# Kernel optimization log

Hardware: AMD Instinct MI355X
Metric: run time of the kernel (lower is better)

## Reference

```python
import jax, jax.numpy as jnp
from jax import lax
import numpy as np

K = 3        # adaptive kernel size
STRIDE = 1
PAD = (K - 1) // 2


def setup_inputs() -> dict:
    key = jax.random.key(0)
    ks = jax.random.split(key, 10)
    N, C, H, W = 32, 512, 56, 56
    Cm, P = 128, 512  # Cm = inplanes // m, P = planes

    def rn(k, shape, scale=0.05):
        return jax.random.normal(k, shape, dtype=jnp.float32) * scale

    return dict(
        x=jax.random.normal(ks[0], (N, C, H, W), dtype=jnp.float32),
        conv_w=rn(ks[1], (Cm, C)),      # self.conv 1x1 weight (squeezed)
        conv_b=rn(ks[2], (Cm,)),        # self.conv bias
        ck_w=rn(ks[3], (K * K,)),       # self.conv_kernel 1x1 weight (1 in-ch)
        ck_b=rn(ks[4], (K * K,)),       # self.conv_kernel bias
        ckk_w=rn(ks[5], (Cm,)),         # self.conv_k 1x1 weight (1 in-ch)
        ckk_b=rn(ks[6], (Cm,)),         # self.conv_k bias
        adap_b=rn(ks[7], (Cm,)),        # self.conv_adap_kernel bias (weight is generated)
        fuse_w=rn(ks[8], (P, Cm)),      # self.fuse 1x1 weight (squeezed)
        fuse_b=rn(ks[9], (P,)),         # self.fuse bias
    )


def _forward(x, conv_w, conv_b, ck_w, ck_b, ckk_w, ckk_b, adap_b, fuse_w, fuse_b):
    N, C, H, W = x.shape
    Cm = conv_w.shape[0]

    # f = relu(conv(x)) : [N, Cm, H, W]
    f = jax.nn.relu(jnp.einsum('nchw,oc->nohw', x, conv_w) + conv_b[None, :, None, None])

    # g = relu(conv(avg_pool(x))) : [N, Cm]  (spatial dims are 1x1, squeezed)
    pooled = jnp.mean(x, axis=(2, 3))                       # [N, C]
    g = jax.nn.relu(pooled @ conv_w.T + conv_b)             # [N, Cm]

    # conv_kernel (1x1, 1->k*k channels) applied on permuted g:
    # ker[n, ic, kk] = ck_w[kk] * g[n, ic] + ck_b[kk]
    ker = g[:, :, None] * ck_w[None, None, :] + ck_b[None, None, :]   # [N, Cm, k*k]

    # conv_k (1x1, 1->Cm channels) generates per-sample dynamic conv weights:
    # Wk[n, oc, ic, kk] = relu(ckk_w[oc] * ker[n, ic, kk] + ckk_b[oc])
    Wk = jax.nn.relu(ckk_w[None, :, None, None] * ker[:, None, :, :]
                     + ckk_b[None, :, None, None])          # [N, Cm, Cm, k*k]
    Wk = Wk.reshape(N, Cm, Cm, K, K)                        # per-sample OIHW weights

    # Per-sample dynamic conv, batched with vmap (replaces the python loop + weight swap)
    def dyn_conv(f_n, w_n):  # f_n: [Cm,H,W], w_n: [Cm,Cm,K,K]
        return lax.conv_general_dilated(
            f_n[None], w_n, (STRIDE, STRIDE), [(PAD, PAD), (PAD, PAD)],
            dimension_numbers=('NCHW', 'OIHW', 'NCHW'))[0]

    y = jax.vmap(dyn_conv)(f, Wk) + adap_b[None, :, None, None]  # [N, Cm, H, W]

    # fuse 1x1 conv: Cm -> planes
    out = jnp.einsum('nchw,pc->nphw', y, fuse_w) + fuse_b[None, :, None, None]
    return out


def reference(x, conv_w, conv_b, ck_w, ck_b, ckk_w, ckk_b, adap_b, fuse_w, fuse_b):
    return _forward(x, conv_w, conv_b, ck_w, ck_b, ckk_w, ckk_b, adap_b, fuse_w, fuse_b)
```

## Files before the change

### kernel.cpp

```cpp
#include <hip/hip_runtime.h>

#define N_   32
#define C_   512
#define HW_  3136
#define W_   56
#define H_   56
#define CM_  128
#define P_   512

typedef __attribute__((ext_vector_type(8))) short bf16x8;
typedef __attribute__((ext_vector_type(4))) float f32x4;

__device__ inline ushort f2bf(float x) {
    unsigned u = __float_as_uint(x);
    u += 0x7fff + ((u >> 16) & 1);
    return (ushort)(u >> 16);
}

__global__ __launch_bounds__(256) void prep_w(const float* __restrict__ conv_w,
                                              const float* __restrict__ fuse_w,
                                              ushort* __restrict__ Acv,
                                              ushort* __restrict__ Afu,
                                              float* __restrict__ gacc) {
    int idx = blockIdx.x * 256 + threadIdx.x;
    if (idx < 4096) gacc[idx] = 0.f;
    if (idx < 65536) {
        int ci = idx & 7, cm = (idx >> 3) & 127, cb = idx >> 10;
        Acv[idx] = f2bf(conv_w[cm * C_ + cb * 8 + ci]);
    } else {
        int j = idx - 65536;
        int ci = j & 7, p = (j >> 3) & 511, kb = j >> 12;
        Afu[j] = f2bf(fuse_w[p * CM_ + kb * 8 + ci]);
    }
}

__global__ __launch_bounds__(256) void gemm_f(const float* __restrict__ x,
                                              const ushort* __restrict__ Acv,
                                              const float* __restrict__ conv_b,
                                              ushort* __restrict__ f_t,
                                              float* __restrict__ gacc) {
    int pixbase = blockIdx.x * 64, n = blockIdx.z;
    int t = threadIdx.x, wv = t >> 6, lane = t & 63, col = lane & 15, quad = lane >> 4;
    __shared__ ushort bsh[2][64 * 40];
    f32x4 z = {0.f, 0.f, 0.f, 0.f};
    f32x4 acc[2][4];
    #pragma unroll
    for (int mt = 0; mt < 2; mt++)
        #pragma unroll
        for (int ns = 0; ns < 4; ns++) acc[mt][ns] = z;

    int spix = t & 63, chq = wv * 8;
    const float* xb = &x[(size_t)n * C_ * HW_ + pixbase + spix];

    float v[8];
#define LOADV(c0)                                                              \
    {                                                                          \
        const float* xs = xb + (size_t)(c0) * HW_;                             \
        _Pragma("unroll")                                                      \
        for (int i = 0; i < 8; i++) v[i] = xs[(size_t)(chq + i) * HW_];        \
    }
#define PACKW(buf)                                                             \
    {                                                                          \
        unsigned p0 = (unsigned)f2bf(v[0]) | ((unsigned)f2bf(v[1]) << 16);     \
        unsigned p1 = (unsigned)f2bf(v[2]) | ((unsigned)f2bf(v[3]) << 16);     \
        unsigned p2 = (unsigned)f2bf(v[4]) | ((unsigned)f2bf(v[5]) << 16);     \
        unsigned p3 = (unsigned)f2bf(v[6]) | ((unsigned)f2bf(v[7]) << 16);     \
        *(uint4*)&bsh[buf][spix * 40 + chq] = make_uint4(p0, p1, p2, p3);      \
    }

    LOADV(0);
    PACKW(0);
    __syncthreads();
    int cur = 0;
    for (int cb0 = 0; cb0 < 16; cb0++) {
        if (cb0 < 15) {
            LOADV((cb0 + 1) * 32);
            PACKW(cur ^ 1);
        }
        bf16x8 a[2], b[4];
        #pragma unroll
        for (int mt = 0; mt < 2; mt++)
            a[mt] = *(const bf16x8*)&Acv[(((cb0 * 4 + quad) * CM_) + wv * 32 + mt * 16 + col) * 8];
        #pragma unroll
        for (int ns = 0; ns < 4; ns++)
            b[ns] = *(const bf16x8*)&bsh[cur][(ns * 16 + col) * 40 + quad * 8];
        #pragma unroll
        for (int mt = 0; mt < 2; mt++)
            #pragma unroll
            for (int ns = 0; ns < 4; ns++)
                acc[mt][ns] = __builtin_amdgcn_mfma_f32_16x16x32_bf16(a[mt], b[ns], acc[mt][ns], 0, 0, 0);
        __syncthreads();
        cur ^= 1;
    }
#undef LOADV
#undef PACKW

    #pragma unroll
    for (int mt = 0; mt < 2; mt++) {
        float ps0 = acc[mt][0][0] + acc[mt][1][0] + acc[mt][2][0] + acc[mt][3][0];
        float ps1 = acc[mt][0][1] + acc[mt][1][1] + acc[mt][2][1] + acc[mt][3][1];
        float ps2 = acc[mt][0][2] + acc[mt][1][2] + acc[mt][2][2] + acc[mt][3][2];
        float ps3 = acc[mt][0][3] + acc[mt][1][3] + acc[mt][2][3] + acc[mt][3][3];
        #pragma unroll
        for (int off = 1; off < 16; off <<= 1) {
            ps0 += __shfl_xor(ps0, off);
            ps1 += __shfl_xor(ps1, off);
            ps2 += __shfl_xor(ps2, off);
            ps3 += __shfl_xor(ps3, off);
        }
        if (col == 0) {
            int ocr = wv * 32 + mt * 16 + quad * 4;
            atomicAdd(&gacc[n * CM_ + ocr],     ps0);
            atomicAdd(&gacc[n * CM_ + ocr + 1], ps1);
            atomicAdd(&gacc[n * CM_ + ocr + 2], ps2);
            atomicAdd(&gacc[n * CM_ + ocr + 3], ps3);
        }
    }

    #pragma unroll
    for (int mt = 0; mt < 2; mt++) {
        int ocr = wv * 32 + mt * 16 + quad * 4;
        float b0 = conv_b[ocr], b1 = conv_b[ocr + 1], b2 = conv_b[ocr + 2], b3 = conv_b[ocr + 3];
        #pragma unroll
        for (int ns = 0; ns < 4; ns++) {
            int pix = pixbase + ns * 16 + col;
            ushort4 o;
            o.x = f2bf(fmaxf(acc[mt][ns][0] + b0, 0.f));
            o.y = f2bf(fmaxf(acc[mt][ns][1] + b1, 0.f));
            o.z = f2bf(fmaxf(acc[mt][ns][2] + b2, 0.f));
            o.w = f2bf(fmaxf(acc[mt][ns][3] + b3, 0.f));
            *(ushort4*)&f_t[((size_t)(n * HW_ + pix)) * CM_ + ocr] = o;
        }
    }
}

__global__ __launch_bounds__(256) void wk_frag(const float* __restrict__ gacc,
                                               const float* __restrict__ conv_b,
                                               const float* __restrict__ ck_w,
                                               const float* __restrict__ ck_b,
                                               const float* __restrict__ ckk_w,
                                               const float* __restrict__ ckk_b,
                                               ushort* __restrict__ Wkf) {
    int idx = blockIdx.x * 256 + threadIdx.x;
    int ci = idx & 7, oc = (idx >> 3) & 127, icb = (idx >> 10) & 15, rest = idx >> 14;
    int kk = rest % 9, n = rest / 9;
    int ic = icb * 8 + ci;
    float gv = fmaxf(gacc[n * CM_ + ic] * (1.0f / (float)HW_) + conv_b[ic], 0.f);
    float ker = ck_w[kk] * gv + ck_b[kk];
    Wkf[idx] = f2bf(fmaxf(ckk_w[oc] * ker + ckk_b[oc], 0.f));
}

__global__ __launch_bounds__(256) void gemm_dyn_fuse(const ushort* __restrict__ f_t,
                                                     const ushort* __restrict__ Wkf,
                                                     const float* __restrict__ adap_b,
                                                     const ushort* __restrict__ Afu,
                                                     const float* __restrict__ fuse_b,
                                                     float* __restrict__ out) {
    int lid = blockIdx.x;
    int j = lid >> 3;
    int n = (lid & 7) + 8 * (j / 49);
    int pixbase = (j % 49) * 64;
    int t = threadIdx.x, wv = t >> 6, lane = t & 63, col = lane & 15, quad = lane >> 4;
    int h_lo = pixbase / W_;
    __shared__ ushort smem[10240];
    ushort* fsh = smem;
    ushort* ysh = smem;
    int ldspix[4];
    #pragma unroll
    for (int ns = 0; ns < 4; ns++) {
        int pix = pixbase + ns * 16 + col;
        int h = pix / W_, w = pix - h * W_;
        ldspix[ns] = (h - h_lo) * 58 + w;
    }
    f32x4 acc[2][4];
    #pragma unroll
    for (int mt = 0; mt < 2; mt++) {
        int ocr = wv * 32 + mt * 16 + quad * 4;
        f32x4 ab = {adap_b[ocr], adap_b[ocr + 1], adap_b[ocr + 2], adap_b[ocr + 3]};
        #pragma unroll
        for (int ns = 0; ns < 4; ns++) acc[mt][ns] = ab;
    }
    for (int ic0 = 0; ic0 < CM_; ic0 += 32) {
        #pragma unroll
        for (int it = 0; it < 4; it++) {
            int idx = it * 256 + t;
            if (idx < 928) {
                int lp = idx >> 2, ch = idx & 3;
                int r = lp / 58, cw = lp - r * 58;
                int hp = h_lo + r;
                uint4 v = {0u, 0u, 0u, 0u};
                if (hp >= 1 && hp <= H_ && cw >= 1 && cw <= W_)
                    v = *(const uint4*)&f_t[((size_t)(n * HW_ + (hp - 1) * W_ + cw - 1)) * CM_ + ic0 + ch * 8];
                *(uint4*)&fsh[lp * 40 + ch * 8] = v;
            }
        }
        __syncthreads();
        #pragma unroll
        for (int dh = 0; dh < 3; dh++) {
            #pragma unroll
            for (int dw = 0; dw < 3; dw++) {
                int kk = dh * 3 + dw;
                bf16x8 a[2], b[4];
                #pragma unroll
                for (int mt = 0; mt < 2; mt++)
                    a[mt] = *(const bf16x8*)&Wkf[((((size_t)(n * 9 + kk) * 16) + (ic0 >> 3) + quad) * CM_ + wv * 32 + mt * 16 + col) * 8];
                #pragma unroll
                for (int ns = 0; ns < 4; ns++)
                    b[ns] = *(const bf16x8*)&fsh[(ldspix[ns] + dh * 58 + dw) * 40 + quad * 8];
                #pragma unroll
                for (int mt = 0; mt < 2; mt++)
                    #pragma unroll
                    for (int ns = 0; ns < 4; ns++)
                        acc[mt][ns] = __builtin_amdgcn_mfma_f32_16x16x32_bf16(a[mt], b[ns], acc[mt][ns], 0, 0, 0);
            }
        }
        __syncthreads();
    }

    #pragma unroll
    for (int mt = 0; mt < 2; mt++) {
        #pragma unroll
        for (int ns = 0; ns < 4; ns++) {
            int lpix = ns * 16 + col;
            ushort4 o;
            o.x = f2bf(acc[mt][ns][0]);
            o.y = f2bf(acc[mt][ns][1]);
            o.z = f2bf(acc[mt][ns][2]);
            o.w = f2bf(acc[mt][ns][3]);
            *(ushort4*)&ysh[wv * 2560 + lpix * 40 + mt * 16 + quad * 4] = o;
        }
    }
    __syncthreads();

    #pragma unroll 1
    for (int pb = 0; pb < 4; pb++) {
        f32x4 z = {0.f, 0.f, 0.f, 0.f};
        f32x4 facc[2][4];
        #pragma unroll
        for (int mt = 0; mt < 2; mt++)
            #pragma unroll
            for (int ns = 0; ns < 4; ns++) facc[mt][ns] = z;
        #pragma unroll
        for (int cb0 = 0; cb0 < 4; cb0++) {
            bf16x8 a[2], b[4];
            #pragma unroll
            for (int mt = 0; mt < 2; mt++)
                a[mt] = *(const bf16x8*)&Afu[(((cb0 * 4 + quad) * P_) + pb * 128 + wv * 32 + mt * 16 + col) * 8];
            #pragma unroll
            for (int ns = 0; ns < 4; ns++)
                b[ns] = *(const bf16x8*)&ysh[cb0 * 2560 + (ns * 16 + col) * 40 + quad * 8];
            #pragma unroll
            for (int mt = 0; mt < 2; mt++)
                #pragma unroll
                for (int ns = 0; ns < 4; ns++)
                    facc[mt][ns] = __builtin_amdgcn_mfma_f32_16x16x32_bf16(a[mt], b[ns], facc[mt][ns], 0, 0, 0);
        }
        #pragma unroll
        for (int mt = 0; mt < 2; mt++) {
            int pr = pb * 128 + wv * 32 + mt * 16 + quad * 4;
            #pragma unroll
            for (int ns = 0; ns < 4; ns++) {
                int pix = pixbase + ns * 16 + col;
                #pragma unroll
                for (int r = 0; r < 4; r++)
                    out[((size_t)(n * P_ + pr + r)) * HW_ + pix] = facc[mt][ns][r] + fuse_b[pr + r];
            }
        }
    }
}

extern "C" void kernel_launch(void* const* d_in, const int* in_sizes, int n_in,
                              void* d_out, int out_size, void* d_ws, size_t ws_size,
                              hipStream_t stream) {
    const float* x      = (const float*)d_in[0];
    const float* conv_w = (const float*)d_in[1];
    const float* conv_b = (const float*)d_in[2];
    const float* ck_w   = (const float*)d_in[3];
    const float* ck_b   = (const float*)d_in[4];
    const float* ckk_w  = (const float*)d_in[5];
    const float* ckk_b  = (const float*)d_in[6];
    const float* adap_b = (const float*)d_in[7];
    const float* fuse_w = (const float*)d_in[8];
    const float* fuse_b = (const float*)d_in[9];
    float* out = (float*)d_out;

    ushort* f_t = (ushort*)d_ws;
    ushort* Wkf = f_t + (size_t)12845056;
    ushort* Acv = Wkf + (size_t)4718592;
    ushort* Afu = Acv + (size_t)65536;
    float* gacc = (float*)(Afu + (size_t)65536);

    prep_w<<<512, 256, 0, stream>>>(conv_w, fuse_w, Acv, Afu, gacc);
    gemm_f<<<dim3(49, 1, N_), 256, 0, stream>>>(x, Acv, conv_b, f_t, gacc);
    wk_frag<<<18432, 256, 0, stream>>>(gacc, conv_b, ck_w, ck_b, ckk_w, ckk_b, Wkf);
    gemm_dyn_fuse<<<dim3(1568), 256, 0, stream>>>(f_t, Wkf, adap_b, Afu, fuse_b, out);
}
```

Baseline: 435.4 us.

## Prefetch next input stage into registers during MFMA compute in both GEMM kernels

In the first 1x1 conv kernel, the bf16 pack into the alternate shared buffer now runs after the MFMAs, so the global loads overlap the compute. In the dynamic conv kernel, the halo-tile addresses are precomputed once and the next 32-channel slice is loaded into registers before the 3x3 MFMA loop. That slice is written to shared memory only after a barrier. This hides global load latency behind compute, at the cost of more live registers and an extra barrier per stage.

```diff
diff --git a/kernel.cpp b/kernel.cpp
--- a/kernel.cpp
+++ b/kernel.cpp
@@ -73,10 +73,7 @@
     __syncthreads();
     int cur = 0;
     for (int cb0 = 0; cb0 < 16; cb0++) {
-        if (cb0 < 15) {
-            LOADV((cb0 + 1) * 32);
-            PACKW(cur ^ 1);
-        }
+        if (cb0 < 15) LOADV((cb0 + 1) * 32);
         bf16x8 a[2], b[4];
         #pragma unroll
         for (int mt = 0; mt < 2; mt++)
@@ -89,6 +86,7 @@
             #pragma unroll
             for (int ns = 0; ns < 4; ns++)
                 acc[mt][ns] = __builtin_amdgcn_mfma_f32_16x16x32_bf16(a[mt], b[ns], acc[mt][ns], 0, 0, 0);
+        if (cb0 < 15) PACKW(cur ^ 1);
         __syncthreads();
         cur ^= 1;
     }
@@ -172,6 +170,37 @@
         int h = pix / W_, w = pix - h * W_;
         ldspix[ns] = (h - h_lo) * 58 + w;
     }
+
+    const ushort* fsrc[4];
+    int ldst[4];
+    bool sval[4];
+    #pragma unroll
+    for (int it = 0; it < 4; it++) {
+        int idx = it * 256 + t;
+        ldst[it] = -1; sval[it] = false; fsrc[it] = f_t;
+        if (idx < 928) {
+            int lp = idx >> 2, ch = idx & 3;
+            int r = lp / 58, cw = lp - r * 58;
+            int hp = h_lo + r;
+            ldst[it] = lp * 40 + ch * 8;
+            if (hp >= 1 && hp <= H_ && cw >= 1 && cw <= W_) {
+                sval[it] = true;
+                fsrc[it] = &f_t[((size_t)(n * HW_ + (hp - 1) * W_ + cw - 1)) * CM_ + ch * 8];
+            }
+        }
+    }
+    uint4 vst[4];
+#define STAGE_LOAD(ic0)                                                        \
+    _Pragma("unroll")                                                          \
+    for (int it = 0; it < 4; it++) {                                           \
+        vst[it] = make_uint4(0u, 0u, 0u, 0u);                                  \
+        if (sval[it]) vst[it] = *(const uint4*)(fsrc[it] + (ic0));             \
+    }
+#define STAGE_WRITE()                                                          \
+    _Pragma("unroll")                                                          \
+    for (int it = 0; it < 4; it++)                                             \
+        if (ldst[it] >= 0) *(uint4*)&fsh[ldst[it]] = vst[it];
+
     f32x4 acc[2][4];
     #pragma unroll
     for (int mt = 0; mt < 2; mt++) {
@@ -180,21 +209,13 @@
         #pragma unroll
         for (int ns = 0; ns < 4; ns++) acc[mt][ns] = ab;
     }
-    for (int ic0 = 0; ic0 < CM_; ic0 += 32) {
-        #pragma unroll
-        for (int it = 0; it < 4; it++) {
-            int idx = it * 256 + t;
-            if (idx < 928) {
-                int lp = idx >> 2, ch = idx & 3;
-                int r = lp / 58, cw = lp - r * 58;
-                int hp = h_lo + r;
-                uint4 v = {0u, 0u, 0u, 0u};
-                if (hp >= 1 && hp <= H_ && cw >= 1 && cw <= W_)
-                    v = *(const uint4*)&f_t[((size_t)(n * HW_ + (hp - 1) * W_ + cw - 1)) * CM_ + ic0 + ch * 8];
-                *(uint4*)&fsh[lp * 40 + ch * 8] = v;
-            }
-        }
-        __syncthreads();
+
+    STAGE_LOAD(0);
+    STAGE_WRITE();
+    __syncthreads();
+    for (int s = 0; s < 4; s++) {
+        int ic0 = s * 32;
+        if (s < 3) STAGE_LOAD(ic0 + 32);
         #pragma unroll
         for (int dh = 0; dh < 3; dh++) {
             #pragma unroll
@@ -215,7 +236,13 @@
             }
         }
         __syncthreads();
-    }
+        if (s < 3) {
+            STAGE_WRITE();
+            __syncthreads();
+        }
+    }
+#undef STAGE_LOAD
+#undef STAGE_WRITE
 
     #pragma unroll
     for (int mt = 0; mt < 2; mt++) {
```

Result: slower. 444.3 us (+2.0%).
